# Kernel tuning notes

Hardware: AMD Instinct MI355X
Metric: run time of the kernel (lower is better)

The kernel has to match this reference:

```python
import jax, jax.numpy as jnp
import numpy as np
from jax import lax

D_MODEL = 1024
D_INNER = 2 * D_MODEL          # expand=2
D_STATE = 16
D_CONV = 4
DT_RANK = 64                   # ceil(1024/16)
DT_MIN = 0.001
DT_MAX = 0.1
BATCH = 4
SEQ = 2048


def setup_inputs() -> dict:
    key = jax.random.key(0)
    ks = jax.random.split(key, 8)
    s = lambda fan_in: 1.0 / np.sqrt(fan_in)
    x = jax.random.normal(ks[0], (BATCH, SEQ, D_MODEL), dtype=jnp.float32)
    # Linear weights stored as (in, out) so y = x @ W
    W_in = jax.random.uniform(ks[1], (D_MODEL, 2 * D_INNER), jnp.float32, -s(D_MODEL), s(D_MODEL))
    conv_w = jax.random.uniform(ks[2], (D_INNER, 1, D_CONV), jnp.float32, -s(D_CONV), s(D_CONV))
    conv_b = jax.random.uniform(ks[3], (D_INNER,), jnp.float32, -s(D_CONV), s(D_CONV))
    W_x = jax.random.uniform(ks[4], (D_INNER, DT_RANK + 2 * D_STATE), jnp.float32, -s(D_INNER), s(D_INNER))
    W_dt = jax.random.uniform(ks[5], (DT_RANK, D_INNER), jnp.float32, -s(DT_RANK), s(DT_RANK))
    b_dt = jax.random.uniform(ks[6], (D_INNER,), jnp.float32, -s(DT_RANK), s(DT_RANK))
    # A = arange(1..d_state) repeated over d_inner; store log(A)
    A_log = jnp.log(jnp.broadcast_to(jnp.arange(1, D_STATE + 1, dtype=jnp.float32), (D_INNER, D_STATE)))
    D_param = jnp.ones((D_INNER,), dtype=jnp.float32)
    W_out = jax.random.uniform(ks[7], (D_INNER, D_MODEL), jnp.float32, -s(D_INNER), s(D_INNER))
    return {"x": x, "W_in": W_in, "conv_w": conv_w, "conv_b": conv_b,
            "W_x": W_x, "W_dt": W_dt, "b_dt": b_dt, "A_log": A_log,
            "D_param": D_param, "W_out": W_out}


def reference(x, W_in, conv_w, conv_b, W_x, W_dt, b_dt, A_log, D_param, W_out):
    # in_proj + split
    xz = x @ W_in                                   # (B, S, 2*d_inner)
    x_branch, z_branch = jnp.split(xz, 2, axis=-1)  # each (B, S, d_inner)

    # causal depthwise conv1d (torch pads d_conv-1 both sides then slices [:seq])
    xc = jnp.pad(x_branch.transpose(0, 2, 1), ((0, 0), (0, 0), (D_CONV - 1, 0)))
    xc = lax.conv_general_dilated(xc, conv_w, (1,), 'VALID',
                                  dimension_numbers=('NCH', 'OIH', 'NCH'),
                                  feature_group_count=D_INNER)
    xc = xc + conv_b[None, :, None]
    x_conv = jax.nn.silu(xc.transpose(0, 2, 1))     # (B, S, d_inner)

    # input-dependent dt, B, C
    x_dbl = x_conv @ W_x                            # (B, S, dt_rank + 2*d_state)
    dt_low = x_dbl[..., :DT_RANK]
    Bm = x_dbl[..., DT_RANK:DT_RANK + D_STATE]      # (B, S, d_state)
    Cm = x_dbl[..., DT_RANK + D_STATE:]             # (B, S, d_state)
    dt = jax.nn.sigmoid(dt_low @ W_dt + b_dt) * (DT_MAX - DT_MIN) + DT_MIN
    dt = jnp.maximum(dt, 1e-4)                      # (B, S, d_inner)

    A = -jnp.exp(A_log)                             # (d_inner, d_state)

    # selective scan over time (n_substeps = 1)
    def step(h, inp):
        dt_t, B_t, C_t, x_t = inp                   # (B,di), (B,ds), (B,ds), (B,di)
        dA = jnp.exp(dt_t[:, :, None] * A[None])    # (B, di, ds)
        h = dA * h + (dt_t * x_t)[:, :, None] * B_t[:, None, :]
        y_t = jnp.sum(h * C_t[:, None, :], axis=-1) # (B, di)
        return h, y_t

    h0 = jnp.zeros((x.shape[0], D_INNER, D_STATE), dtype=x.dtype)
    _, ys = lax.scan(step, h0,
                     (dt.swapaxes(0, 1), Bm.swapaxes(0, 1),
                      Cm.swapaxes(0, 1), x_conv.swapaxes(0, 1)))
    y = ys.swapaxes(0, 1)                           # (B, S, d_inner)

    y = y + x_conv * D_param
    y = y * jax.nn.silu(z_branch)
    return y @ W_out                                # (B, S, d_model)
```

## Files before the change

kernel.cpp:

```cpp
#include <hip/hip_runtime.h>

typedef unsigned short u16;
typedef unsigned int u32;
typedef __attribute__((ext_vector_type(8))) short short8;
typedef __attribute__((ext_vector_type(4))) short short4v;
typedef __attribute__((ext_vector_type(2))) short short2v;
typedef __attribute__((ext_vector_type(4))) float f32x4;

#define NBATCH 4
#define NSEQ   2048
#define DMODEL 1024
#define DINNER 2048
#define DSTATE 16
#define DTRANK 64
#define ROWS   (NBATCH*NSEQ)
#define NCH    64
#define CLEN   32

__device__ __forceinline__ float b2f(u16 u){ union{u32 i; float f;} v; v.i=((u32)u)<<16; return v.f; }
__device__ __forceinline__ u16 f2b(float f){ union{float f; u32 i;} v; v.f=f; u32 i=v.i; return (u16)((i + 0x7FFFu + ((i>>16)&1u))>>16); }
__device__ __forceinline__ float sigmoidf_(float x){ return 1.0f/(1.0f+__expf(-x)); }

__device__ __forceinline__ void pow16(float e1, float (&pw)[16]){
  float p2 = e1*e1, p4 = p2*p2, p8 = p4*p4;
  pw[0]=e1;        pw[1]=p2;        pw[2]=e1*p2;     pw[3]=p4;
  pw[4]=e1*p4;     pw[5]=p2*p4;     pw[6]=pw[2]*p4;  pw[7]=p8;
  pw[8]=e1*p8;     pw[9]=p2*p8;     pw[10]=pw[2]*p8; pw[11]=p4*p8;
  pw[12]=pw[4]*p8; pw[13]=pw[5]*p8; pw[14]=pw[6]*p8; pw[15]=p8*p8;
}

__global__ __launch_bounds__(256) void prep(const u16* __restrict__ x,
    const u16* __restrict__ Win, const u16* __restrict__ convw,
    const u16* __restrict__ Wx, const u16* __restrict__ Wdt,
    const u16* __restrict__ Alog, const u16* __restrict__ Wout,
    const u16* __restrict__ v0, const u16* __restrict__ v1, const u16* __restrict__ v2,
    int* __restrict__ meta){
  __shared__ int vote;
  __shared__ int mxbits;
  const int tid = threadIdx.x;
  const u16* V[3] = {v0, v1, v2};

  const u16* ptrs[6] = {x, Win, convw, Wx, Wdt, Wout};
  const float bounds[6] = {8.f, 0.045f, 0.6f, 0.035f, 0.15f, 0.035f};
  const int slots[6] = {0, 1, 2, 4, 5, 9};
  for (int q = 0; q < 6; q++){
    if (tid == 0) vote = 1;
    __syncthreads();
    int bad = 0;
    for (int i = tid; i < 2048; i += 256){
      float v = fabsf(b2f(ptrs[q][i]));
      if (!(v <= bounds[q])) bad = 1;
    }
    if (bad) atomicAnd(&vote, 0);
    __syncthreads();
    if (tid == 0) meta[slots[q]] = vote;
    __syncthreads();
  }
  if (tid == 0){ u16 u = Alog[1]; meta[7] = (u == 0x3F31 || u == 0x3F32) ? 1 : 0; }

  int iD = -1, fD = 1;
  for (int k = 0; k < 3; k++){
    if (V[k][0] == 0x3F80 && V[k][1] == 0x3F80){ iD = k; fD = 1; }
    else if (V[k][0] == 0 && V[k][1] == 0x3F80 && V[k][2] == 0){ iD = k; fD = 0; }
  }
  if (iD < 0){ iD = 2; fD = 1; }
  int oo[2], no = 0;
  for (int k = 0; k < 3; k++) if (k != iD) oo[no++] = k;
  int fo[2]; float mo[2];
  for (int q = 0; q < 2; q++){
    if (tid == 0) vote = 1;
    __syncthreads();
    int bad = 0;
    for (int i = tid; i < 2048; i += 256){
      float v = fabsf(b2f(V[oo[q]][i]));
      if (!(v <= 0.6f)) bad = 1;
    }
    if (bad) atomicAnd(&vote, 0);
    __syncthreads();
    fo[q] = vote;
    if (tid == 0) mxbits = 0;
    __syncthreads();
    float m = 0.f;
    for (int i = tid; i < 2048; i += 256){
      float v = fabsf(fo[q] ? b2f(V[oo[q]][i]) : ((const float*)V[oo[q]])[i]);
      m = fmaxf(m, v);
    }
    atomicMax(&mxbits, __float_as_int(m));
    __syncthreads();
    mo[q] = __int_as_float(mxbits);
    __syncthreads();
  }
  if (tid == 0){
    int a = (mo[0] > 0.25f) ? 0 : 1;
    meta[10] = oo[a];     meta[3] = fo[a];
    meta[11] = oo[1-a];   meta[6] = fo[1-a];
    meta[12] = iD;        meta[8] = fD;
  }
}

__global__ __launch_bounds__(256) void cvt_bf16(const void* __restrict__ in,
                                                u16* __restrict__ out, long n,
                                                const int* __restrict__ meta, int slot){
  long i = (long)blockIdx.x*256 + threadIdx.x;
  if (i >= n) return;
  if (meta[slot]) out[i] = ((const u16*)in)[i];
  else            out[i] = f2b(((const float*)in)[i]);
}

__global__ __launch_bounds__(256) void cvt_x8(const void* __restrict__ in,
                                              u16* __restrict__ out,
                                              const int* __restrict__ meta){
  long i8 = ((long)blockIdx.x*256 + threadIdx.x)*8;
  if (meta[0]){
    *(short8*)(out + i8) = *(const short8*)((const u16*)in + i8);
  } else {
    const float* f = (const float*)in + i8;
    f32x4 a = *(const f32x4*)f;
    f32x4 b = *(const f32x4*)(f+4);
    short8 o;
    #pragma unroll
    for (int j=0;j<4;j++){ ((u16*)&o)[j] = f2b(a[j]); ((u16*)&o)[4+j] = f2b(b[j]); }
    *(short8*)(out + i8) = o;
  }
}

__global__ __launch_bounds__(256) void cvt_trio(const void* __restrict__ v0,
                                                const void* __restrict__ v1,
                                                const void* __restrict__ v2,
                                                const int* __restrict__ meta,
                                                u16* __restrict__ cbc,
                                                u16* __restrict__ bdtc,
                                                u16* __restrict__ dpc){
  int i = blockIdx.x*256 + threadIdx.x;
  int which = i >> 11, d = i & 2047;
  const void* V[3] = {v0, v1, v2};
  int src, fl; u16* dst;
  if (which == 0){ src = meta[10]; fl = meta[3]; dst = cbc; }
  else if (which == 1){ src = meta[11]; fl = meta[6]; dst = bdtc; }
  else { src = meta[12]; fl = meta[8]; dst = dpc; }
  dst[d] = fl ? ((const u16*)V[src])[d] : f2b(((const float*)V[src])[d]);
}

__global__ __launch_bounds__(256) void transpose_pad(const void* __restrict__ inv,
                                                     u16* __restrict__ out,
                                                     int K, int N, int Nout,
                                                     const int* __restrict__ meta, int slot){
  __shared__ u16 t[32][33];
  const int f = meta[slot];
  const u16*   ib = (const u16*)inv;
  const float* iff = (const float*)inv;
  int k0 = blockIdx.x*32, n0 = blockIdx.y*32;
  int tx = threadIdx.x & 31, ty = threadIdx.x >> 5;
  #pragma unroll
  for (int i=0;i<32;i+=8){
    int k = k0+ty+i, n = n0+tx;
    u16 v = 0;
    if (k<K && n<N) v = f ? ib[(long)k*N+n] : f2b(iff[(long)k*N+n]);
    t[ty+i][tx] = v;
  }
  __syncthreads();
  #pragma unroll
  for (int i=0;i<32;i+=8){
    int n = n0+ty+i, k = k0+tx;
    if (n<Nout && k<K) out[(long)n*K+k] = t[tx][ty+i];
  }
}

template<int MODE>
__global__ __launch_bounds__(256) void gemm_bt(
    const u16* __restrict__ A, int lda,
    const u16* __restrict__ Bt, int K,
    u16* __restrict__ C0, u16* __restrict__ C1, int ldc,
    const u16* __restrict__ bias, float* __restrict__ Cf)
{
  __shared__ u16 sa[128*64];
  __shared__ u16 sb[128*64];
  const int tid = threadIdx.x;
  const int lane = tid & 63;
  const int wave = tid >> 6;
  const int wm = (wave >> 1) * 64;
  const int wn = (wave & 1) * 64;
  const int lane15 = lane & 15;
  const int quad = lane >> 4;
  const long rowBase = (long)blockIdx.y * 128;
  const long colBase = (long)blockIdx.x * 128;

  int kbeg = 0, kend = K;
  if (MODE == 4){
    const int span = K >> 2;
    kbeg = blockIdx.z * span;
    kend = kbeg + span;
    Cf += (long)blockIdx.z * (8192L*128);
  }

  f32x4 acc[4][4];
  #pragma unroll
  for (int i=0;i<4;i++)
    #pragma unroll
    for (int j=0;j<4;j++)
      #pragma unroll
      for (int r=0;r<4;r++) acc[i][j][r]=0.0f;

  const int e  = tid*8;
  const int r0 = e >> 6;
  const int c0 = e & 63;

  for (int kb=kbeg; kb<kend; kb+=64) {
    #pragma unroll
    for (int i=0;i<4;i++){
      const u16* ga = A + (rowBase + r0 + i*32)*lda + kb + c0;
      __builtin_amdgcn_global_load_lds((const __attribute__((address_space(1))) void*)ga,
                                       (__attribute__((address_space(3))) void*)&sa[e + i*2048],
                                       16, 0, 0);
    }
    #pragma unroll
    for (int i=0;i<4;i++){
      const u16* gb = Bt + (colBase + r0 + i*32)*(long)K + kb + c0;
      __builtin_amdgcn_global_load_lds((const __attribute__((address_space(1))) void*)gb,
                                       (__attribute__((address_space(3))) void*)&sb[e + i*2048],
                                       16, 0, 0);
    }
    __syncthreads();
    #pragma unroll
    for (int ko=0; ko<2; ko++){
      const int kk = ko*32 + quad*8;
      short8 af[4], bfr[4];
      #pragma unroll
      for (int i=0;i<4;i++) af[i]  = *(const short8*)&sa[(wm + i*16 + lane15)*64 + kk];
      #pragma unroll
      for (int j=0;j<4;j++) bfr[j] = *(const short8*)&sb[(wn + j*16 + lane15)*64 + kk];
      #pragma unroll
      for (int i=0;i<4;i++)
        #pragma unroll
        for (int j=0;j<4;j++)
          acc[i][j] = __builtin_amdgcn_mfma_f32_16x16x32_bf16(af[i], bfr[j], acc[i][j], 0, 0, 0);
    }
    __syncthreads();
  }

  #pragma unroll
  for (int i=0;i<4;i++){
    #pragma unroll
    for (int j=0;j<4;j++){
      long row = rowBase + wm + i*16 + quad*4;
      long col = colBase + wn + j*16 + lane15;
      #pragma unroll
      for (int r=0;r<4;r++){
        float v = acc[i][j][r];
        long rr = row + r;
        if (MODE == 0) {
          C0[rr*ldc + col] = f2b(v);
        } else if (MODE == 2) {
          float t  = sigmoidf_(v + b2f(bias[col]));
          float dv = fmaxf(t*0.099f + 0.001f, 1e-4f);
          C0[rr*ldc + col] = f2b(dv);
        } else if (MODE == 3 || MODE == 4) {
          Cf[rr*ldc + col] = v;
        }
      }
    }
  }
}

__global__ __launch_bounds__(256) void reduce_xdbl(const float* __restrict__ P,
                                                   u16* __restrict__ out){
  const long i4 = ((long)blockIdx.x*256 + threadIdx.x)*4;
  f32x4 a = *(const f32x4*)(P + i4);
  f32x4 b = *(const f32x4*)(P + 1048576 + i4);
  f32x4 c = *(const f32x4*)(P + 2097152 + i4);
  f32x4 d = *(const f32x4*)(P + 3145728 + i4);
  short4v o;
  #pragma unroll
  for (int j=0;j<4;j++) ((u16*)&o)[j] = f2b(a[j]+b[j]+c[j]+d[j]);
  *(short4v*)(out + i4) = o;
}

template<int MODE>
__global__ __launch_bounds__(512, 2) void gemm256(
    const u16* __restrict__ A, int lda,
    const u16* __restrict__ Bt, int K,
    u16* __restrict__ C0, u16* __restrict__ C1, int ldc,
    float* __restrict__ Cf)
{
  __shared__ u16 sa[2*16384];
  __shared__ u16 sb[2*16384];
  const int tid  = threadIdx.x;
  const int lane = tid & 63;
  const int wm   = (tid >> 6) >> 2;
  const int wn   = (tid >> 6) & 3;
  const int lane15 = lane & 15;
  const int quad   = lane >> 4;

  const int nwg  = gridDim.x * gridDim.y;
  const int orig = blockIdx.y * gridDim.x + blockIdx.x;
  const int swz  = (orig & 7) * (nwg >> 3) + (orig >> 3);
  const int bx   = swz % gridDim.x;
  const int by   = swz / gridDim.x;
  const long rowBase = (long)by * 256;
  const long colBase = (long)bx * 256;

  const int xorv = (lane15 & 7) << 3;
  const int k0   = (quad*8) ^ xorv;
  const int k1   = (32 + quad*8) ^ xorv;
  const int aBase = (wm*128 + lane15) * 64;
  const int bBase = (wn*64  + lane15) * 64;

  const int scol = ((tid & 7) ^ ((tid >> 3) & 7)) << 3;
  const int arow = tid >> 3;
  const int bsub = ((tid >> 8) & 1)*64 + ((tid & 255) >> 3);
  const int bdst = (tid & 7) * 8;

  f32x4 acc[8][4];
  #pragma unroll
  for (int i=0;i<8;i++)
    #pragma unroll
    for (int j=0;j<4;j++)
      #pragma unroll
      for (int r=0;r<4;r++) acc[i][j][r]=0.0f;

  const int nt = K >> 6;

  auto stageA = [&](int buf, int rs, int kb){
    const u16* g = A + (rowBase + rs + arow)*(long)lda + kb + scol;
    __builtin_amdgcn_global_load_lds((const __attribute__((address_space(1))) void*)g,
        (__attribute__((address_space(3))) void*)&sa[buf*16384 + rs*64 + tid*8], 16, 0, 0);
  };
  auto stageB = [&](int buf, int cq, int part, int kb){
    const int row = part*128 + cq*32 + bsub;
    const u16* g = Bt + (colBase + row)*(long)K + kb + scol;
    __builtin_amdgcn_global_load_lds((const __attribute__((address_space(1))) void*)g,
        (__attribute__((address_space(3))) void*)&sb[buf*16384 + row*64 + bdst], 16, 0, 0);
  };

  stageA(0,   0, 0); stageA(0, 128, 0);
  stageB(0, 0, 0, 0); stageB(0, 0, 1, 0);
  stageA(0,  64, 0); stageA(0, 192, 0);
  stageB(0, 1, 0, 0); stageB(0, 1, 1, 0);
  asm volatile("s_waitcnt vmcnt(4)\n\ts_barrier" ::: "memory");

  for (int t = 0; t < nt; ++t){
    const int cur = t & 1, nb = cur ^ 1;
    const int kb2 = (t+1) << 6;
    const bool pf = (t+1 < nt);
    const u16* sA = &sa[cur*16384];
    const u16* sB = &sb[cur*16384];
    short8 a0[4][2], a1[4][2], b0[2][2], b1[2][2];

    #pragma unroll
    for (int i=0;i<4;i++){
      a0[i][0] = *(const short8*)&sA[aBase + i*1024 + k0];
      a0[i][1] = *(const short8*)&sA[aBase + i*1024 + k1];
    }
    #pragma unroll
    for (int j=0;j<2;j++){
      b0[j][0] = *(const short8*)&sB[bBase + j*1024 + k0];
      b0[j][1] = *(const short8*)&sB[bBase + j*1024 + k1];
    }
    if (pf){ stageA(nb, 0, kb2); stageA(nb, 128, kb2); }
    __builtin_amdgcn_s_setprio(1);
    #pragma unroll
    for (int s=0;s<2;s++)
      #pragma unroll
      for (int i=0;i<4;i++)
        #pragma unroll
        for (int j=0;j<2;j++)
          acc[i][j] = __builtin_amdgcn_mfma_f32_16x16x32_bf16(a0[i][s], b0[j][s], acc[i][j], 0, 0, 0);
    __builtin_amdgcn_s_setprio(0);
    asm volatile("s_waitcnt vmcnt(4)\n\ts_barrier" ::: "memory");

    #pragma unroll
    for (int i=0;i<4;i++){
      a1[i][0] = *(const short8*)&sA[aBase + 4096 + i*1024 + k0];
      a1[i][1] = *(const short8*)&sA[aBase + 4096 + i*1024 + k1];
    }
    if (pf){ stageB(nb, 0, 0, kb2); stageB(nb, 0, 1, kb2); }
    __builtin_amdgcn_s_setprio(1);
    #pragma unroll
    for (int s=0;s<2;s++)
      #pragma unroll
      for (int i=0;i<4;i++)
        #pragma unroll
        for (int j=0;j<2;j++)
          acc[4+i][j] = __builtin_amdgcn_mfma_f32_16x16x32_bf16(a1[i][s], b0[j][s], acc[4+i][j], 0, 0, 0);
    __builtin_amdgcn_s_setprio(0);
    asm volatile("s_waitcnt vmcnt(4)\n\ts_barrier" ::: "memory");

    #pragma unroll
    for (int j=0;j<2;j++){
      b1[j][0] = *(const short8*)&sB[bBase + 2048 + j*1024 + k0];
      b1[j][1] = *(const short8*)&sB[bBase + 2048 + j*1024 + k1];
    }
    if (pf){ stageA(nb, 64, kb2); stageA(nb, 192, kb2); }
    __builtin_amdgcn_s_setprio(1);
    #pragma unroll
    for (int s=0;s<2;s++)
      #pragma unroll
      for (int i=0;i<4;i++)
        #pragma unroll
        for (int j=0;j<2;j++)
          acc[i][2+j] = __builtin_amdgcn_mfma_f32_16x16x32_bf16(a0[i][s], b1[j][s], acc[i][2+j], 0, 0, 0);
    __builtin_amdgcn_s_setprio(0);
    asm volatile("s_barrier" ::: "memory");

    if (pf){ stageB(nb, 1, 0, kb2); stageB(nb, 1, 1, kb2); }
    __builtin_amdgcn_s_setprio(1);
    #pragma unroll
    for (int s=0;s<2;s++)
      #pragma unroll
      for (int i=0;i<4;i++)
        #pragma unroll
        for (int j=0;j<2;j++)
          acc[4+i][2+j] = __builtin_amdgcn_mfma_f32_16x16x32_bf16(a1[i][s], b1[j][s], acc[4+i][2+j], 0, 0, 0);
    __builtin_amdgcn_s_setprio(0);
    asm volatile("s_waitcnt vmcnt(4)\n\ts_barrier" ::: "memory");
  }

  #pragma unroll
  for (int i=0;i<8;i++){
    const long row = rowBase + wm*128 + i*16 + quad*4;
    #pragma unroll
    for (int j=0;j<4;j++){
      const long col = colBase + wn*64 + j*16 + lane15;
      #pragma unroll
      for (int r=0;r<4;r++){
        const float v = acc[i][j][r];
        const long rr = row + r;
        if (MODE == 1){
          if (col < 2048) C0[rr*2048 + col] = f2b(v);
          else            C1[rr*2048 + (col-2048)] = f2b(v);
        } else {
          Cf[rr*ldc + col] = v;
        }
      }
    }
  }
}

__global__ __launch_bounds__(256) void conv_silu(const u16* __restrict__ xb,
                                                 const u16* __restrict__ w,
                                                 const u16* __restrict__ bias,
                                                 u16* __restrict__ xc){
  long idx8 = ((long)blockIdx.x*256 + threadIdx.x) * 8;
  int d = (int)(idx8 & (DINNER-1));
  int s = (int)((idx8 >> 11) & (NSEQ-1));
  int b = (int)(idx8 >> 22);

  short8 bv = *(const short8*)(bias + d);
  short8 wv0 = *(const short8*)(w + d*4);
  short8 wv1 = *(const short8*)(w + d*4 + 8);
  short8 wv2 = *(const short8*)(w + d*4 + 16);
  short8 wv3 = *(const short8*)(w + d*4 + 24);
  u16 wl[32];
  #pragma unroll
  for (int q=0;q<8;q++){ wl[q] = ((u16*)&wv0)[q]; wl[8+q] = ((u16*)&wv1)[q];
                         wl[16+q] = ((u16*)&wv2)[q]; wl[24+q] = ((u16*)&wv3)[q]; }

  float acc[8];
  #pragma unroll
  for (int l=0;l<8;l++) acc[l] = b2f(((u16*)&bv)[l]);

  #pragma unroll
  for (int j=0;j<4;j++){
    int t = s - 3 + j;
    if (t >= 0){
      short8 xv = *(const short8*)(xb + ((long)(b*NSEQ + t))*DINNER + d);
      #pragma unroll
      for (int l=0;l<8;l++)
        acc[l] += b2f(((u16*)&xv)[l]) * b2f(wl[l*4 + j]);
    }
  }
  short8 ov;
  #pragma unroll
  for (int l=0;l<8;l++){ float y = acc[l]*sigmoidf_(acc[l]); ((u16*)&ov)[l] = f2b(y); }
  *(short8*)(xc + idx8) = ov;
}

__global__ __launch_bounds__(256) void scan_pass1(const u16* __restrict__ dt,
                                                  const u16* __restrict__ xc,
                                                  const u16* __restrict__ xdbl,
                                                  const u16* __restrict__ Alog,
                                                  float* __restrict__ hend,
                                                  float* __restrict__ sumdt){
  const int tid = threadIdx.x;
  const int d0 = blockIdx.x*512 + tid*2;
  const int c = blockIdx.y;
  const int b = blockIdx.z;
  __shared__ float sB[CLEN][DSTATE];
  for (int i=tid; i<CLEN*DSTATE; i+=256){
    int t = i >> 4, s = i & 15;
    sB[t][s] = b2f(xdbl[((long)(b*NSEQ + c*CLEN + t))*128 + DTRANK + s]);
  }
  bool fast = true;
  #pragma unroll
  for (int j=0;j<2;j++)
    #pragma unroll
    for (int s=0;s<DSTATE;s++){
      float a = -__expf(b2f(Alog[(d0+j)*DSTATE + s]));
      fast = fast && (fabsf(a + (float)(s+1)) < 0.03f*(float)(s+1));
    }
  __syncthreads();

  float h[2][DSTATE];
  #pragma unroll
  for (int j=0;j<2;j++)
    #pragma unroll
    for (int s=0;s<DSTATE;s++) h[j][s] = 0.0f;
  float sd[2] = {0.f,0.f};
  long base = ((long)(b*NSEQ + c*CLEN))*DINNER + d0;
  short2v dt2 = *(const short2v*)(dt + base);
  short2v x2  = *(const short2v*)(xc + base);
  if (fast){
    for (int t=0;t<CLEN;t++){
      long nxt = base + (long)((t+1<CLEN)?(t+1):t)*DINNER;
      short2v dtn = *(const short2v*)(dt + nxt);
      short2v xn  = *(const short2v*)(xc + nxt);
      float B[DSTATE];
      *(f32x4*)&B[0]  = *(const f32x4*)&sB[t][0];
      *(f32x4*)&B[4]  = *(const f32x4*)&sB[t][4];
      *(f32x4*)&B[8]  = *(const f32x4*)&sB[t][8];
      *(f32x4*)&B[12] = *(const f32x4*)&sB[t][12];
      #pragma unroll
      for (int j=0;j<2;j++){
        float dtv = b2f(((u16*)&dt2)[j]);
        float xv  = b2f(((u16*)&x2)[j]);
        float u = dtv*xv;
        sd[j] += dtv;
        float e1 = __expf(-dtv);
        float pw[16];
        pow16(e1, pw);
        #pragma unroll
        for (int s=0;s<DSTATE;s++)
          h[j][s] = fmaf(pw[s], h[j][s], u*B[s]);
      }
      dt2 = dtn; x2 = xn;
    }
  } else {
    float Acf[2][DSTATE];
    #pragma unroll
    for (int j=0;j<2;j++)
      #pragma unroll
      for (int s=0;s<DSTATE;s++) Acf[j][s] = -__expf(b2f(Alog[(d0+j)*DSTATE + s]));
    for (int t=0;t<CLEN;t++){
      long nxt = base + (long)((t+1<CLEN)?(t+1):t)*DINNER;
      short2v dtn = *(const short2v*)(dt + nxt);
      short2v xn  = *(const short2v*)(xc + nxt);
      float B[DSTATE];
      *(f32x4*)&B[0]  = *(const f32x4*)&sB[t][0];
      *(f32x4*)&B[4]  = *(const f32x4*)&sB[t][4];
      *(f32x4*)&B[8]  = *(const f32x4*)&sB[t][8];
      *(f32x4*)&B[12] = *(const f32x4*)&sB[t][12];
      #pragma unroll
      for (int j=0;j<2;j++){
        float dtv = b2f(((u16*)&dt2)[j]);
        float xv  = b2f(((u16*)&x2)[j]);
        float u = dtv*xv;
        sd[j] += dtv;
        #pragma unroll
        for (int s=0;s<DSTATE;s++){
          float dA = __expf(dtv * Acf[j][s]);
          h[j][s] = fmaf(dA, h[j][s], u*B[s]);
        }
      }
      dt2 = dtn; x2 = xn;
    }
  }
  #pragma unroll
  for (int j=0;j<2;j++){
    long hidx = ((long)(b*DINNER + d0 + j)*NCH + c)*DSTATE;
    #pragma unroll
    for (int q=0;q<4;q++) *(f32x4*)&hend[hidx + q*4] = *(const f32x4*)&h[j][q*4];
    sumdt[(long)(b*DINNER + d0 + j)*NCH + c] = sd[j];
  }
}

__global__ __launch_bounds__(256) void scan_pass2(float* __restrict__ hend,
                                                  const float* __restrict__ sumdt,
                                                  const u16* __restrict__ Alog){
  long i = (long)blockIdx.x*256 + threadIdx.x;
  int s = (int)(i & 15);
  long bd = i >> 4;
  int d = (int)(bd & (DINNER-1));
  float A = -__expf(b2f(Alog[d*DSTATE + s]));
  float run = 0.0f;
  long base = bd*NCH*DSTATE + s;
  for (int c=0;c<NCH;c++){
    float e = hend[base + (long)c*DSTATE];
    float decay = __expf(A * sumdt[bd*NCH + c]);
    hend[base + (long)c*DSTATE] = run;
    run = run*decay + e;
  }
}

__global__ __launch_bounds__(256) void scan_pass3(const u16* __restrict__ dt,
                                                  u16* __restrict__ xc,
                                                  const u16* __restrict__ zb,
                                                  const u16* __restrict__ xdbl,
                                                  const u16* __restrict__ Alog,
                                                  const u16* __restrict__ Dp,
                                                  const float* __restrict__ hstart){
  const int tid = threadIdx.x;
  const int d0 = blockIdx.x*512 + tid*2;
  const int c = blockIdx.y;
  const int b = blockIdx.z;
  __shared__ float sB[CLEN][DSTATE];
  __shared__ float sC[CLEN][DSTATE];
  for (int i=tid; i<CLEN*DSTATE; i+=256){
    int t = i >> 4, s = i & 15;
    long rb = ((long)(b*NSEQ + c*CLEN + t))*128;
    sB[t][s] = b2f(xdbl[rb + DTRANK + s]);
    sC[t][s] = b2f(xdbl[rb + DTRANK + DSTATE + s]);
  }
  bool fast = true;
  #pragma unroll
  for (int j=0;j<2;j++)
    #pragma unroll
    for (int s=0;s<DSTATE;s++){
      float a = -__expf(b2f(Alog[(d0+j)*DSTATE + s]));
      fast = fast && (fabsf(a + (float)(s+1)) < 0.03f*(float)(s+1));
    }
  __syncthreads();

  float h[2][DSTATE];
  #pragma unroll
  for (int j=0;j<2;j++){
    long hidx = ((long)(b*DINNER + d0 + j)*NCH + c)*DSTATE;
    #pragma unroll
    for (int q=0;q<4;q++) *(f32x4*)&h[j][q*4] = *(const f32x4*)&hstart[hidx + q*4];
  }
  short2v dp2 = *(const short2v*)(Dp + d0);
  long base = ((long)(b*NSEQ + c*CLEN))*DINNER + d0;
  short2v dt2 = *(const short2v*)(dt + base);
  short2v x2  = *(const short2v*)(xc + base);
  short2v z2  = *(const short2v*)(zb + base);
  if (fast){
    for (int t=0;t<CLEN;t++){
      long nxt = base + (long)((t+1<CLEN)?(t+1):t)*DINNER;
      short2v dtn = *(const short2v*)(dt + nxt);
      short2v xn  = *(const short2v*)(xc + nxt);
      short2v zn  = *(const short2v*)(zb + nxt);
      float B[DSTATE], C[DSTATE];
      *(f32x4*)&B[0]  = *(const f32x4*)&sB[t][0];
      *(f32x4*)&B[4]  = *(const f32x4*)&sB[t][4];
      *(f32x4*)&B[8]  = *(const f32x4*)&sB[t][8];
      *(f32x4*)&B[12] = *(const f32x4*)&sB[t][12];
      *(f32x4*)&C[0]  = *(const f32x4*)&sC[t][0];
      *(f32x4*)&C[4]  = *(const f32x4*)&sC[t][4];
      *(f32x4*)&C[8]  = *(const f32x4*)&sC[t][8];
      *(f32x4*)&C[12] = *(const f32x4*)&sC[t][12];
      short2v ov;
      #pragma unroll
      for (int j=0;j<2;j++){
        float dtv = b2f(((u16*)&dt2)[j]);
        float xv  = b2f(((u16*)&x2)[j]);
        float zv  = b2f(((u16*)&z2)[j]);
        float u = dtv*xv;
        float e1 = __expf(-dtv);
        float gate = zv*sigmoidf_(zv);
        float pw[16];
        pow16(e1, pw);
        float y0=0.f, y1=0.f, y2=0.f, y3=0.f;
        #pragma unroll
        for (int q=0;q<4;q++){
          h[j][q*4+0] = fmaf(pw[q*4+0], h[j][q*4+0], u*B[q*4+0]);
          h[j][q*4+1] = fmaf(pw[q*4+1], h[j][q*4+1], u*B[q*4+1]);
          h[j][q*4+2] = fmaf(pw[q*4+2], h[j][q*4+2], u*B[q*4+2]);
          h[j][q*4+3] = fmaf(pw[q*4+3], h[j][q*4+3], u*B[q*4+3]);
          y0 = fmaf(h[j][q*4+0], C[q*4+0], y0);
          y1 = fmaf(h[j][q*4+1], C[q*4+1], y1);
          y2 = fmaf(h[j][q*4+2], C[q*4+2], y2);
          y3 = fmaf(h[j][q*4+3], C[q*4+3], y3);
        }
        float y = (y0+y1)+(y2+y3);
        y = fmaf(xv, b2f(((u16*)&dp2)[j]), y);
        y *= gate;
        ((u16*)&ov)[j] = f2b(y);
      }
      *(short2v*)(xc + base + (long)t*DINNER) = ov;
      dt2 = dtn; x2 = xn; z2 = zn;
    }
  } else {
    float Acf[2][DSTATE];
    #pragma unroll
    for (int j=0;j<2;j++)
      #pragma unroll
      for (int s=0;s<DSTATE;s++) Acf[j][s] = -__expf(b2f(Alog[(d0+j)*DSTATE + s]));
    for (int t=0;t<CLEN;t++){
      long nxt = base + (long)((t+1<CLEN)?(t+1):t)*DINNER;
      short2v dtn = *(const short2v*)(dt + nxt);
      short2v xn  = *(const short2v*)(xc + nxt);
      short2v zn  = *(const short2v*)(zb + nxt);
      float B[DSTATE], C[DSTATE];
      *(f32x4*)&B[0]  = *(const f32x4*)&sB[t][0];
      *(f32x4*)&B[4]  = *(const f32x4*)&sB[t][4];
      *(f32x4*)&B[8]  = *(const f32x4*)&sB[t][8];
      *(f32x4*)&B[12] = *(const f32x4*)&sB[t][12];
      *(f32x4*)&C[0]  = *(const f32x4*)&sC[t][0];
      *(f32x4*)&C[4]  = *(const f32x4*)&sC[t][4];
      *(f32x4*)&C[8]  = *(const f32x4*)&sC[t][8];
      *(f32x4*)&C[12] = *(const f32x4*)&sC[t][12];
      short2v ov;
      #pragma unroll
      for (int j=0;j<2;j++){
        float dtv = b2f(((u16*)&dt2)[j]);
        float xv  = b2f(((u16*)&x2)[j]);
        float zv  = b2f(((u16*)&z2)[j]);
        float u = dtv*xv;
        float gate = zv*sigmoidf_(zv);
        float y = 0.0f;
        #pragma unroll
        for (int s=0;s<DSTATE;s++){
          float dA = __expf(dtv * Acf[j][s]);
          h[j][s] = fmaf(dA, h[j][s], u*B[s]);
          y = fmaf(h[j][s], C[s], y);
        }
        y = fmaf(xv, b2f(((u16*)&dp2)[j]), y);
        y *= gate;
        ((u16*)&ov)[j] = f2b(y);
      }
      *(short2v*)(xc + base + (long)t*DINNER) = ov;
      dt2 = dtn; x2 = xn; z2 = zn;
    }
  }
}

extern "C" void kernel_launch(void* const* d_in, const int* in_sizes, int n_in,
                              void* d_out, int out_size, void* d_ws, size_t ws_size,
                              hipStream_t stream) {
  const void *x=nullptr,*W_in=nullptr,*conv_w=nullptr,*W_x=nullptr,*W_dt=nullptr,
             *A_log=nullptr,*W_out=nullptr;
  const void* v2048[3] = {nullptr,nullptr,nullptr};
  int n2048 = 0;
  for (int i = 0; i < n_in; i++){
    switch (in_sizes[i]){
      case 8388608: x      = d_in[i]; break;
      case 4194304: W_in   = d_in[i]; break;
      case 8192:    conv_w = d_in[i]; break;
      case 196608:  W_x    = d_in[i]; break;
      case 131072:  W_dt   = d_in[i]; break;
      case 32768:   A_log  = d_in[i]; break;
      case 2097152: W_out  = d_in[i]; break;
      case 2048:    if (n2048 < 3) v2048[n2048++] = d_in[i]; break;
      default: break;
    }
  }

  size_t off = 0;
  char* wsb = (char*)d_ws;
  auto take = [&](size_t n){ void* p = wsb + off; off += (n + 255) & ~(size_t)255; return p; };
  u16* Wt_in  = (u16*)take((size_t)4096*1024*2);
  u16* Wt_x   = (u16*)take((size_t)128*2048*2);
  u16* Wt_dt  = (u16*)take((size_t)2048*64*2);
  u16* Wt_out = (u16*)take((size_t)1024*2048*2);
  u16* xb     = (u16*)take((size_t)ROWS*DINNER*2);
  u16* zb     = (u16*)take((size_t)ROWS*DINNER*2);
  u16* xc     = (u16*)take((size_t)ROWS*DINNER*2);
  u16* xdbl   = (u16*)take((size_t)ROWS*128*2);
  char* shr = (char*)take((size_t)ROWS*NCH*DSTATE*4 + (size_t)ROWS*NCH*4 + 4096);
  u16*   xcvt  = (u16*)shr;
  float* hend  = (float*)shr;
  float* sumdt = (float*)(shr + (size_t)ROWS*NCH*DSTATE*4);
  u16* cwc  = (u16*)take(DINNER*4*2);
  u16* cbc  = (u16*)take(DINNER*2);
  u16* bdtc = (u16*)take(DINNER*2);
  u16* alc  = (u16*)take(DINNER*DSTATE*2);
  u16* dpc  = (u16*)take(DINNER*2);
  int* meta = (int*)take(256);
  float* xdp = (float*)take((size_t)4*8192*128*4);
  u16* dtb = xb;

  prep<<<1, 256, 0, stream>>>((const u16*)x, (const u16*)W_in, (const u16*)conv_w,
                              (const u16*)W_x, (const u16*)W_dt, (const u16*)A_log,
                              (const u16*)W_out,
                              (const u16*)v2048[0], (const u16*)v2048[1], (const u16*)v2048[2],
                              meta);

  cvt_x8<<<(ROWS*DMODEL)/(256*8), 256, 0, stream>>>(x, xcvt, meta);
  cvt_bf16<<<32, 256, 0, stream>>>(conv_w, cwc, DINNER*4, meta, 2);
  cvt_bf16<<<128,256, 0, stream>>>(A_log, alc, DINNER*DSTATE, meta, 7);
  cvt_trio<<<24, 256, 0, stream>>>(v2048[0], v2048[1], v2048[2], meta, cbc, bdtc, dpc);

  transpose_pad<<<dim3(32,128), 256, 0, stream>>>(W_in, Wt_in, 1024, 4096, 4096, meta, 1);
  transpose_pad<<<dim3(64,4),   256, 0, stream>>>(W_x,  Wt_x,  2048, 96,   128,  meta, 4);
  transpose_pad<<<dim3(2,64),   256, 0, stream>>>(W_dt, Wt_dt, 64,   2048, 2048, meta, 5);
  transpose_pad<<<dim3(64,32),  256, 0, stream>>>(W_out,Wt_out,2048, 1024, 1024, meta, 9);

  gemm256<1><<<dim3(16,32), 512, 0, stream>>>(xcvt, 1024, Wt_in, 1024, xb, zb, 2048, nullptr);

  conv_silu<<<(ROWS*DINNER)/(256*8), 256, 0, stream>>>(xb, cwc, cbc, xc);

  gemm_bt<4><<<dim3(1,64,4), 256, 0, stream>>>(xc, 2048, Wt_x, 2048, nullptr, nullptr, 128, nullptr, xdp);
  reduce_xdbl<<<1024, 256, 0, stream>>>(xdp, xdbl);

  gemm_bt<2><<<dim3(16,64), 256, 0, stream>>>(xdbl, 128, Wt_dt, 64, dtb, nullptr, 2048, bdtc, nullptr);

  scan_pass1<<<dim3(4,NCH,NBATCH), 256, 0, stream>>>(dtb, xc, xdbl, alc, hend, sumdt);
  scan_pass2<<<(ROWS*DSTATE)/256, 256, 0, stream>>>(hend, sumdt, alc);
  scan_pass3<<<dim3(4,NCH,NBATCH), 256, 0, stream>>>(dtb, xc, zb, xdbl, alc, dpc, hend);

  gemm_bt<3><<<dim3(8,64), 256, 0, stream>>>(xc, 2048, Wt_out, 2048, nullptr, nullptr, 1024, nullptr, (float*)d_out);
}
```

Baseline: 466.8 us.

## Add dedicated 256x128 out-projection GEMM and multi-timestep conv kernel

Replaces the generic gemm_bt<3> out-projection with a new gemm_out kernel. It uses 512 threads, 256x128 tiles, direct global-to-LDS loads, double buffering with split prefetch, workgroup swizzling and MFMA priority hints. The conv+SiLU kernel now computes four consecutive timesteps per thread from seven loaded rows, so overlapping input rows are read once instead of four times. The larger GEMM tile yields only 256 workgroups and raises register and LDS pressure.

```diff
diff --git a/kernel.cpp b/kernel.cpp
--- a/kernel.cpp
+++ b/kernel.cpp
@@ -254,7 +254,7 @@
           float t  = sigmoidf_(v + b2f(bias[col]));
           float dv = fmaxf(t*0.099f + 0.001f, 1e-4f);
           C0[rr*ldc + col] = f2b(dv);
-        } else if (MODE == 3 || MODE == 4) {
+        } else if (MODE == 4) {
           Cf[rr*ldc + col] = v;
         }
       }
@@ -436,14 +436,133 @@
   }
 }
 
-__global__ __launch_bounds__(256) void conv_silu(const u16* __restrict__ xb,
-                                                 const u16* __restrict__ w,
-                                                 const u16* __restrict__ bias,
-                                                 u16* __restrict__ xc){
-  long idx8 = ((long)blockIdx.x*256 + threadIdx.x) * 8;
-  int d = (int)(idx8 & (DINNER-1));
-  int s = (int)((idx8 >> 11) & (NSEQ-1));
-  int b = (int)(idx8 >> 22);
+__global__ __launch_bounds__(512, 2) void gemm_out(
+    const u16* __restrict__ A, int lda,
+    const u16* __restrict__ Bt, int K,
+    float* __restrict__ Cf, int ldc)
+{
+  __shared__ u16 sa[2*16384];
+  __shared__ u16 sb[2*8192];
+  const int tid  = threadIdx.x;
+  const int lane = tid & 63;
+  const int wm   = (tid >> 6) >> 2;
+  const int wn   = (tid >> 6) & 3;
+  const int lane15 = lane & 15;
+  const int quad   = lane >> 4;
+
+  const int nwg  = gridDim.x * gridDim.y;
+  const int orig = blockIdx.y * gridDim.x + blockIdx.x;
+  const int swz  = (orig & 7) * (nwg >> 3) + (orig >> 3);
+  const int bx   = swz % gridDim.x;
+  const int by   = swz / gridDim.x;
+  const long rowBase = (long)by * 256;
+  const long colBase = (long)bx * 128;
+
+  const int xorv = (lane15 & 7) << 3;
+  const int k0   = (quad*8) ^ xorv;
+  const int k1   = (32 + quad*8) ^ xorv;
+  const int aBase = (wm*128 + lane15) * 64;
+  const int bBase = (wn*32  + lane15) * 64;
+
+  const int scol = ((tid & 7) ^ ((tid >> 3) & 7)) << 3;
+  const int arow = tid >> 3;
+
+  f32x4 acc[8][2];
+  #pragma unroll
+  for (int i=0;i<8;i++)
+    #pragma unroll
+    for (int j=0;j<2;j++)
+      #pragma unroll
+      for (int r=0;r<4;r++) acc[i][j][r]=0.0f;
+
+  const int nt = K >> 6;
+
+  auto stageA = [&](int buf, int rs, int kb){
+    const u16* g = A + (rowBase + rs + arow)*(long)lda + kb + scol;
+    __builtin_amdgcn_global_load_lds((const __attribute__((address_space(1))) void*)g,
+        (__attribute__((address_space(3))) void*)&sa[buf*16384 + rs*64 + tid*8], 16, 0, 0);
+  };
+  auto stageB = [&](int buf, int rs, int kb){
+    const u16* g = Bt + (colBase + rs + arow)*(long)K + kb + scol;
+    __builtin_amdgcn_global_load_lds((const __attribute__((address_space(1))) void*)g,
+        (__attribute__((address_space(3))) void*)&sb[buf*8192 + rs*64 + tid*8], 16, 0, 0);
+  };
+
+  stageA(0,0,0); stageA(0,128,0); stageB(0,0,0); stageB(0,64,0);
+  stageA(0,64,0); stageA(0,192,0);
+  asm volatile("s_waitcnt vmcnt(0)\n\ts_barrier" ::: "memory");
+
+  for (int t = 0; t < nt; ++t){
+    const int cur = t & 1, nb = cur ^ 1;
+    const int kb2 = (t+1) << 6;
+    const bool pf = (t+1 < nt);
+    const u16* sA = &sa[cur*16384];
+    const u16* sB = &sb[cur*8192];
+    short8 a0[4][2], a1[4][2], bf_[2][2];
+
+    #pragma unroll
+    for (int i=0;i<4;i++){
+      a0[i][0] = *(const short8*)&sA[aBase + i*1024 + k0];
+      a0[i][1] = *(const short8*)&sA[aBase + i*1024 + k1];
+    }
+    #pragma unroll
+    for (int j=0;j<2;j++){
+      bf_[j][0] = *(const short8*)&sB[bBase + j*1024 + k0];
+      bf_[j][1] = *(const short8*)&sB[bBase + j*1024 + k1];
+    }
+    if (pf){ stageA(nb,0,kb2); stageA(nb,128,kb2); stageB(nb,0,kb2); stageB(nb,64,kb2); }
+    __builtin_amdgcn_s_setprio(1);
+    #pragma unroll
+    for (int s=0;s<2;s++)
+      #pragma unroll
+      for (int i=0;i<4;i++)
+        #pragma unroll
+        for (int j=0;j<2;j++)
+          acc[i][j] = __builtin_amdgcn_mfma_f32_16x16x32_bf16(a0[i][s], bf_[j][s], acc[i][j], 0, 0, 0);
+    __builtin_amdgcn_s_setprio(0);
+    asm volatile("s_waitcnt vmcnt(4)\n\ts_barrier" ::: "memory");
+
+    #pragma unroll
+    for (int i=0;i<4;i++){
+      a1[i][0] = *(const short8*)&sA[aBase + 4096 + i*1024 + k0];
+      a1[i][1] = *(const short8*)&sA[aBase + 4096 + i*1024 + k1];
+    }
+    if (pf){ stageA(nb,64,kb2); stageA(nb,192,kb2); }
+    __builtin_amdgcn_s_setprio(1);
+    #pragma unroll
+    for (int s=0;s<2;s++)
+      #pragma unroll
+      for (int i=0;i<4;i++)
+        #pragma unroll
+        for (int j=0;j<2;j++)
+          acc[4+i][j] = __builtin_amdgcn_mfma_f32_16x16x32_bf16(a1[i][s], bf_[j][s], acc[4+i][j], 0, 0, 0);
+    __builtin_amdgcn_s_setprio(0);
+    asm volatile("s_waitcnt vmcnt(2)\n\ts_barrier" ::: "memory");
+  }
+
+  #pragma unroll
+  for (int i=0;i<8;i++){
+    const long row = rowBase + wm*128 + i*16 + quad*4;
+    #pragma unroll
+    for (int j=0;j<2;j++){
+      const long col = colBase + wn*32 + j*16 + lane15;
+      #pragma unroll
+      for (int r=0;r<4;r++)
+        Cf[(row + r)*ldc + col] = acc[i][j][r];
+    }
+  }
+}
+
+__global__ __launch_bounds__(256) void conv_silu4(const u16* __restrict__ xb,
+                                                  const u16* __restrict__ w,
+                                                  const u16* __restrict__ bias,
+                                                  u16* __restrict__ xc){
+  const int idx = blockIdx.x*256 + threadIdx.x;
+  const int dg = idx & 255;
+  const int sg = (idx >> 8) & 511;
+  const int b  = idx >> 17;
+  const int d  = dg*8;
+  const int s0 = sg*4;
 
   short8 bv = *(const short8*)(bias + d);
   short8 wv0 = *(const short8*)(w + d*4);
@@ -455,24 +574,34 @@
   for (int q=0;q<8;q++){ wl[q] = ((u16*)&wv0)[q]; wl[8+q] = ((u16*)&wv1)[q];
                          wl[16+q] = ((u16*)&wv2)[q]; wl[24+q] = ((u16*)&wv3)[q]; }
 
-  float acc[8];
-  #pragma unroll
-  for (int l=0;l<8;l++) acc[l] = b2f(((u16*)&bv)[l]);
-
-  #pragma unroll
-  for (int j=0;j<4;j++){
-    int t = s - 3 + j;
-    if (t >= 0){
-      short8 xv = *(const short8*)(xb + ((long)(b*NSEQ + t))*DINNER + d);
+  short8 xr[7];
+  #pragma unroll
+  for (int q=0;q<7;q++){
+    int t = s0 - 3 + q;
+    short8 z;
+    #pragma unroll
+    for (int l=0;l<8;l++) ((u16*)&z)[l] = 0;
+    if (t >= 0) z = *(const short8*)(xb + ((long)(b*NSEQ + t))*DINNER + d);
+    xr[q] = z;
+  }
+
+  #pragma unroll
+  for (int st=0; st<4; st++){
+    float acc[8];
+    #pragma unroll
+    for (int l=0;l<8;l++) acc[l] = b2f(((u16*)&bv)[l]);
+    #pragma unroll
+    for (int j=0;j<4;j++){
+      const short8& xv = xr[st + j];
       #pragma unroll
       for (int l=0;l<8;l++)
         acc[l] += b2f(((u16*)&xv)[l]) * b2f(wl[l*4 + j]);
     }
-  }
-  short8 ov;
-  #pragma unroll
-  for (int l=0;l<8;l++){ float y = acc[l]*sigmoidf_(acc[l]); ((u16*)&ov)[l] = f2b(y); }
-  *(short8*)(xc + idx8) = ov;
+    short8 ov;
+    #pragma unroll
+    for (int l=0;l<8;l++){ float y = acc[l]*sigmoidf_(acc[l]); ((u16*)&ov)[l] = f2b(y); }
+    *(short8*)(xc + ((long)(b*NSEQ + s0 + st))*DINNER + d) = ov;
+  }
 }
 
 __global__ __launch_bounds__(256) void scan_pass1(const u16* __restrict__ dt,
@@ -786,7 +915,7 @@
 
   gemm256<1><<<dim3(16,32), 512, 0, stream>>>(xcvt, 1024, Wt_in, 1024, xb, zb, 2048, nullptr);
 
-  conv_silu<<<(ROWS*DINNER)/(256*8), 256, 0, stream>>>(xb, cwc, cbc, xc);
+  conv_silu4<<<(ROWS*DINNER)/(256*32), 256, 0, stream>>>(xb, cwc, cbc, xc);
 
   gemm_bt<4><<<dim3(1,64,4), 256, 0, stream>>>(xc, 2048, Wt_x, 2048, nullptr, nullptr, 128, nullptr, xdp);
   reduce_xdbl<<<1024, 256, 0, stream>>>(xdp, xdbl);
@@ -797,5 +926,5 @@
   scan_pass2<<<(ROWS*DSTATE)/256, 256, 0, stream>>>(hend, sumdt, alc);
   scan_pass3<<<dim3(4,NCH,NBATCH), 256, 0, stream>>>(dtb, xc, zb, xdbl, alc, dpc, hend);
 
-  gemm_bt<3><<<dim3(8,64), 256, 0, stream>>>(xc, 2048, Wt_out, 2048, nullptr, nullptr, 1024, nullptr, (float*)d_out);
-}
+  gemm_out<<<dim3(8,32), 512, 0, stream>>>(xc, 2048, Wt_out, 2048, (float*)d_out, 1024);
+}
```

Measured after the change: 444.6 us, median of 2. 1.05x faster.
